# Optimization experiments

Hardware: AMD Instinct MI355X
Metric: run time of the kernel (lower is better)

Reference implementation:

```python
import jax, jax.numpy as jnp
import numpy as np

B, L, D, H, DK, DV, FF, V, N = 1, 1024, 1024, 16, 64, 64, 4096, 32000, 12


def _ln(x, s, b):
    mu = jnp.mean(x, axis=-1, keepdims=True)
    var = jnp.mean((x - mu) ** 2, axis=-1, keepdims=True)
    return (x - mu) / jnp.sqrt(var + 1e-5) * s + b


def _pe(length, d):
    # interleaved sin/cos positional encoding, matching stack([sin,cos],-1).view(L,D)
    i = 2.0 * jnp.arange(d // 2, dtype=jnp.float32)
    base = 10000.0 ** (-i / d)
    half = jnp.arange(length, dtype=jnp.float32)[:, None] * base[None, :]  # [L, D/2]
    return jnp.stack([jnp.sin(half), jnp.cos(half)], axis=-1).reshape(length, d)


def setup_inputs() -> dict:
    key = jax.random.key(0)
    ks = jax.random.split(key, 8)
    s = 0.02
    return {
        "tokens": jax.random.randint(ks[0], (B, L), 0, V),
        "emb": jax.random.normal(ks[1], (V, D), jnp.float32) * s,
        "final_b": jnp.zeros((V,), jnp.float32),
        "Wq": jax.random.normal(ks[2], (N, H, D, DK), jnp.float32) * s,
        "Wk": jax.random.normal(ks[3], (N, H, D, DK), jnp.float32) * s,
        "Wv": jax.random.normal(ks[4], (N, H, D, DV), jnp.float32) * s,
        "Wo": jax.random.normal(ks[5], (N, H * DV, D), jnp.float32) * s,
        "ln1_s": jnp.ones((N, D), jnp.float32),
        "ln1_b": jnp.zeros((N, D), jnp.float32),
        "W1": jax.random.normal(ks[6], (N, D, FF), jnp.float32) * s,
        "b1": jnp.zeros((N, FF), jnp.float32),
        "W2": jax.random.normal(ks[7], (N, FF, D), jnp.float32) * s,
        "b2": jnp.zeros((N, D), jnp.float32),
        "ln2_s": jnp.ones((N, D), jnp.float32),
        "ln2_b": jnp.zeros((N, D), jnp.float32),
    }


def _forward(tokens, emb, final_b, Wq, Wk, Wv, Wo, ln1_s, ln1_b, W1, b1, W2, b2, ln2_s, ln2_b):
    a = emb[tokens] * jnp.sqrt(jnp.float32(3.0 * D))  # tied-weight scaling
    a = a + (a + _pe(L, D))  # faithful to `a += pe(a)` where pe returns x + PE
    mask = jnp.tril(jnp.ones((L, L), dtype=bool))
    scale = 1.0 / jnp.sqrt(jnp.float32(D))  # original divides by sqrt(d_model), not d_k

    def layer(x, p):
        wq, wk, wv, wo, s1, sb1, w1, bb1, w2, bb2, s2, sb2 = p
        q = jnp.einsum('bld,hdk->bhlk', x, wq)
        k = jnp.einsum('bld,hdk->bhlk', x, wk)
        v = jnp.einsum('bld,hdv->bhlv', x, wv)
        scores = jnp.einsum('bhqk,bhmk->bhqm', q, k) * scale  # [B,H,L,L]
        scores = jnp.where(mask, scores, -jnp.inf)  # causal triu(-inf)
        attn = jax.nn.softmax(scores, axis=-1)
        o = jnp.einsum('bhqm,bhmv->bhqv', attn, v)
        o = o.transpose(0, 2, 1, 3).reshape(x.shape[0], L, H * DV)  # concat heads
        x = _ln(x + o @ wo, s1, sb1)  # post-LN residual
        f = jax.nn.relu(x @ w1 + bb1) @ w2 + bb2
        x = _ln(x + f, s2, sb2)
        return x, None

    x, _ = jax.lax.scan(layer, a, (Wq, Wk, Wv, Wo, ln1_s, ln1_b, W1, b1, W2, b2, ln2_s, ln2_b))
    return x @ emb.T + final_b  # tied output projection with bias


def reference(tokens, emb, final_b, Wq, Wk, Wv, Wo, ln1_s, ln1_b, W1, b1, W2, b2, ln2_s, ln2_b):
    return _forward(tokens, emb, final_b, Wq, Wk, Wv, Wo, ln1_s, ln1_b, W1, b1, W2, b2, ln2_s, ln2_b)
```

## Files before the change

### kernel.cpp

```cpp
#include <hip/hip_runtime.h>

typedef unsigned short u16;
typedef __attribute__((ext_vector_type(8))) short short8;
typedef __attribute__((ext_vector_type(4))) float f32x4;
typedef __attribute__((ext_vector_type(4))) u16 u16x4;

#define LSEQ   1024
#define DMODEL 1024
#define NHEAD  16
#define DHEAD  64
#define DFF    4096
#define NLAYER 12
#define NVOCAB 32000

__device__ __forceinline__ u16 f2b(float f) {
  union { float f; unsigned u; } x; x.f = f;
  unsigned r = x.u + 0x7fffu + ((x.u >> 16) & 1u);
  return (u16)(r >> 16);
}

__device__ __forceinline__ f32x4 mfma16(short8 a, short8 b, f32x4 c) {
  return __builtin_amdgcn_mfma_f32_16x16x32_bf16(a, b, c, 0, 0, 0);
}

__device__ __forceinline__ void gload16(const u16* g, u16* l) {
  __builtin_amdgcn_global_load_lds(
      (const __attribute__((address_space(1))) void*)g,
      (__attribute__((address_space(3))) void*)l, 16, 0, 0);
}

template<int N> __device__ __forceinline__ void waitvm() {
  if constexpr (N <= 0)      asm volatile("s_waitcnt vmcnt(0)" ::: "memory");
  else if constexpr (N == 1) asm volatile("s_waitcnt vmcnt(1)" ::: "memory");
  else if constexpr (N == 2) asm volatile("s_waitcnt vmcnt(2)" ::: "memory");
  else if constexpr (N == 3) asm volatile("s_waitcnt vmcnt(3)" ::: "memory");
  else if constexpr (N == 4) asm volatile("s_waitcnt vmcnt(4)" ::: "memory");
  else if constexpr (N == 5) asm volatile("s_waitcnt vmcnt(5)" ::: "memory");
  else if constexpr (N == 6) asm volatile("s_waitcnt vmcnt(6)" ::: "memory");
  else                       asm volatile("s_waitcnt vmcnt(8)" ::: "memory");
}

__global__ __launch_bounds__(256) void embed_k(const int* __restrict__ tok,
    const float* __restrict__ emb, float* __restrict__ x, u16* __restrict__ xb)
{
  const int l = blockIdx.x;
  const int d0 = threadIdx.x * 4;
  const int t = tok[l];
  const float lf = (float)l;
  float o[4]; u16 obv[4];
#pragma unroll
  for (int j = 0; j < 4; ++j) {
    int d = d0 + j;
    int p = d >> 1;
    float ang = lf * powf(10000.0f, -(float)(2 * p) / 1024.0f);
    float pe = (d & 1) ? cosf(ang) : sinf(ang);
    float val = 2.0f * emb[(size_t)t * DMODEL + d] * 55.42562584220407f + pe;
    o[j] = val; obv[j] = f2b(val);
  }
  *reinterpret_cast<float4*>(x + (size_t)l * DMODEL + d0) = make_float4(o[0], o[1], o[2], o[3]);
  u16x4 vb = { obv[0], obv[1], obv[2], obv[3] };
  *reinterpret_cast<u16x4*>(xb + (size_t)l * DMODEL + d0) = vb;
}

__global__ __launch_bounds__(256) void ln_k(const float* __restrict__ xin,
    const float* __restrict__ ypart, int P, const float* __restrict__ ybias,
    const float* __restrict__ s, const float* __restrict__ b,
    float* __restrict__ xout, u16* __restrict__ xbout)
{
  const int row = blockIdx.x, tid = threadIdx.x;
  const int d0 = tid * 4;
  float4 xv = *reinterpret_cast<const float4*>(xin + (size_t)row * DMODEL + d0);
  float t0 = xv.x, t1 = xv.y, t2 = xv.z, t3 = xv.w;
#pragma unroll 2
  for (int p = 0; p < P; ++p) {
    float4 yv = *reinterpret_cast<const float4*>(ypart + (size_t)p * (LSEQ * DMODEL) + (size_t)row * DMODEL + d0);
    t0 += yv.x; t1 += yv.y; t2 += yv.z; t3 += yv.w;
  }
  if (ybias) {
    float4 bb = *reinterpret_cast<const float4*>(ybias + d0);
    t0 += bb.x; t1 += bb.y; t2 += bb.z; t3 += bb.w;
  }
  float sum = t0 + t1 + t2 + t3;
  float sq  = t0 * t0 + t1 * t1 + t2 * t2 + t3 * t3;
#pragma unroll
  for (int d = 1; d < 64; d <<= 1) { sum += __shfl_xor(sum, d); sq += __shfl_xor(sq, d); }
  __shared__ float ssum[4], ssq[4];
  const int wid = tid >> 6;
  if ((tid & 63) == 0) { ssum[wid] = sum; ssq[wid] = sq; }
  __syncthreads();
  sum = ssum[0] + ssum[1] + ssum[2] + ssum[3];
  sq  = ssq[0] + ssq[1] + ssq[2] + ssq[3];
  const float mu = sum * (1.0f / 1024.0f);
  const float var = sq * (1.0f / 1024.0f) - mu * mu;
  const float rstd = rsqrtf(var + 1e-5f);
  float4 sv = *reinterpret_cast<const float4*>(s + d0);
  float4 bv = *reinterpret_cast<const float4*>(b + d0);
  float o0 = (t0 - mu) * rstd * sv.x + bv.x;
  float o1 = (t1 - mu) * rstd * sv.y + bv.y;
  float o2 = (t2 - mu) * rstd * sv.z + bv.z;
  float o3 = (t3 - mu) * rstd * sv.w + bv.w;
  *reinterpret_cast<float4*>(xout + (size_t)row * DMODEL + d0) = make_float4(o0, o1, o2, o3);
  u16x4 vb = { f2b(o0), f2b(o1), f2b(o2), f2b(o3) };
  *reinterpret_cast<u16x4*>(xbout + (size_t)row * DMODEL + d0) = vb;
}

__global__ __launch_bounds__(256) void tconv_k(const float* __restrict__ in, u16* __restrict__ out,
                                               int R, int C, int zper, int lstride, int obase, int zstride)
{
  __shared__ float t[64][65];
  const int rt = blockIdx.y * 64, ct = blockIdx.x * 64;
  const int z = blockIdx.z;
  in += (size_t)z * zstride;
  const int tr = threadIdx.x >> 4, tc = threadIdx.x & 15;
#pragma unroll
  for (int i = 0; i < 4; ++i) {
    int r = i * 16 + tr;
    float4 v = *reinterpret_cast<const float4*>(in + (size_t)(rt + r) * C + ct + tc * 4);
    t[r][tc * 4 + 0] = v.x; t[r][tc * 4 + 1] = v.y;
    t[r][tc * 4 + 2] = v.z; t[r][tc * 4 + 3] = v.w;
  }
  __syncthreads();
  const size_t orow0 = (size_t)(z / zper) * lstride + (size_t)(z % zper) * C + obase + ct;
#pragma unroll
  for (int i = 0; i < 4; ++i) {
    int c = i * 16 + tr;
    u16x4 o;
    o[0] = f2b(t[tc * 4 + 0][c]); o[1] = f2b(t[tc * 4 + 1][c]);
    o[2] = f2b(t[tc * 4 + 2][c]); o[3] = f2b(t[tc * 4 + 3][c]);
    *reinterpret_cast<u16x4*>(out + (orow0 + c) * R + rt + tc * 4) = o;
  }
}

__global__ __launch_bounds__(256) void ec_k(const float* __restrict__ in, u16* __restrict__ out)
{
  const size_t i = ((size_t)blockIdx.x * 256 + threadIdx.x) * 8;
  float4 a = *reinterpret_cast<const float4*>(in + i);
  float4 b = *reinterpret_cast<const float4*>(in + i + 4);
  short8 o;
  o[0] = f2b(a.x); o[1] = f2b(a.y); o[2] = f2b(a.z); o[3] = f2b(a.w);
  o[4] = f2b(b.x); o[5] = f2b(b.y); o[6] = f2b(b.z); o[7] = f2b(b.w);
  *reinterpret_cast<short8*>(out + i) = o;
}

template<int BM, int BN, int BK, int BSRC, bool BIAS, bool RELU, int OUTMODE, int KSPLIT>
__global__ __launch_bounds__(256) void gemm_bt(
    const u16* __restrict__ A, int lda,
    const void* __restrict__ Bp, int ldb,
    const float* __restrict__ bias,
    void* __restrict__ Cv, int ldc, int Ktot)
{
  constexpr int CPR = BK / 8;
  constexpr int SWM = CPR - 1;
  constexpr int LA = (BM * CPR) / 256;
  constexpr int LB = (BN * CPR) / 256;
  constexpr int LT = LA + LB;
  __shared__ u16 As[3][BM * BK];
  __shared__ u16 Bs[3][BN * BK];
  const int tid = threadIdx.x, lane = tid & 63, wid = tid >> 6;
  const int nwg = gridDim.x * gridDim.y;
  const int flat = blockIdx.y * gridDim.x + blockIdx.x;
  const int qq = nwg >> 3;
  const int ni = (flat & 7) * qq + (flat >> 3);
  const int m0 = (ni % gridDim.x) * BM, n0 = (ni / gridDim.x) * BN;
  const int kbase = (KSPLIT > 1) ? blockIdx.z * (Ktot / KSPLIT) : 0;
  const int klen  = (KSPLIT > 1) ? (Ktot / KSPLIT) : Ktot;
  constexpr int FM = BM / 32, FN = BN / 32;
  constexpr int KS = BK / 32;
  const int wm = (wid >> 1) * (BM / 2), wn = (wid & 1) * (BN / 2);
  f32x4 acc[FM][FN] = {};

  if constexpr (BSRC == 0) {
    const u16* Bt = (const u16*)Bp;
    auto stage = [&](int slot, int k0) {
#pragma unroll
      for (int i = 0; i < LA; ++i) {
        int c = i * 256 + tid;
        int row = c / CPR, p0 = c % CPR;
        int part = p0 ^ (((row * CPR) >> 3) & SWM);
        gload16(A + (size_t)(m0 + row) * lda + k0 + part * 8,
                &As[slot][(i * 256 + wid * 64) * 8]);
      }
#pragma unroll
      for (int i = 0; i < LB; ++i) {
        int c = i * 256 + tid;
        int row = c / CPR, p0 = c % CPR;
        int part = p0 ^ (((row * CPR) >> 3) & SWM);
        gload16(Bt + (size_t)(n0 + row) * ldb + k0 + part * 8,
                &Bs[slot][(i * 256 + wid * 64) * 8]);
      }
    };

    const int NT = klen / BK;
    stage(0, kbase);
    stage(1, kbase + BK);
    waitvm<LT>();
    __builtin_amdgcn_s_barrier();
    asm volatile("" ::: "memory");

    int cur = 0, stg = 2;
    for (int t = 0; t < NT; ++t) {
      const bool more = (t + 2 < NT);
      if (more) stage(stg, kbase + (t + 2) * BK);
      asm volatile("" ::: "memory");
      short8 a[KS][FM], b[KS][FN];
#pragma unroll
      for (int ks = 0; ks < KS; ++ks) {
#pragma unroll
        for (int fm = 0; fm < FM; ++fm) {
          int row = wm + fm * 16 + (lane & 15);
          int pidx = (ks * 4 + (lane >> 4)) ^ (((row * CPR) >> 3) & SWM);
          a[ks][fm] = *reinterpret_cast<const short8*>(&As[cur][row * BK + pidx * 8]);
        }
#pragma unroll
        for (int fn = 0; fn < FN; ++fn) {
          int row = wn + fn * 16 + (lane & 15);
          int pidx = (ks * 4 + (lane >> 4)) ^ (((row * CPR) >> 3) & SWM);
          b[ks][fn] = *reinterpret_cast<const short8*>(&Bs[cur][row * BK + pidx * 8]);
        }
      }
#pragma unroll
      for (int ks = 0; ks < KS; ++ks)
#pragma unroll
        for (int fm = 0; fm < FM; ++fm)
#pragma unroll
          for (int fn = 0; fn < FN; ++fn)
            acc[fm][fn] = mfma16(a[ks][fm], b[ks][fn], acc[fm][fn]);
      if (more) waitvm<LT>(); else waitvm<0>();
      __builtin_amdgcn_s_barrier();
      asm volatile("" ::: "memory");
      cur = (cur == 2) ? 0 : cur + 1;
      stg = (stg == 2) ? 0 : stg + 1;
    }
  } else {
    const float* Bf = (const float*)Bp;
    for (int k0 = 0; k0 < Ktot; k0 += BK) {
#pragma unroll
      for (int i = 0; i < LA; ++i) {
        int c = i * 256 + tid;
        int row = c / CPR, part = c % CPR;
        gload16(A + (size_t)(m0 + row) * lda + k0 + part * 8,
                &As[0][(i * 256 + wid * 64) * 8]);
      }
      {
        int row = tid >> 1, kh = (tid & 1) * 16;
        const float* src = Bf + (size_t)(n0 + row) * ldb + k0 + kh;
        float4 v0 = *reinterpret_cast<const float4*>(src);
        float4 v1 = *reinterpret_cast<const float4*>(src + 4);
        float4 v2 = *reinterpret_cast<const float4*>(src + 8);
        float4 v3 = *reinterpret_cast<const float4*>(src + 12);
        short8 p0, p1;
        p0[0] = f2b(v0.x); p0[1] = f2b(v0.y); p0[2] = f2b(v0.z); p0[3] = f2b(v0.w);
        p0[4] = f2b(v1.x); p0[5] = f2b(v1.y); p0[6] = f2b(v1.z); p0[7] = f2b(v1.w);
        p1[0] = f2b(v2.x); p1[1] = f2b(v2.y); p1[2] = f2b(v2.z); p1[3] = f2b(v2.w);
        p1[4] = f2b(v3.x); p1[5] = f2b(v3.y); p1[6] = f2b(v3.z); p1[7] = f2b(v3.w);
        *reinterpret_cast<short8*>(&Bs[0][row * BK + kh])     = p0;
        *reinterpret_cast<short8*>(&Bs[0][row * BK + kh + 8]) = p1;
      }
      __syncthreads();
      short8 a[KS][FM], b[KS][FN];
#pragma unroll
      for (int ks = 0; ks < KS; ++ks) {
#pragma unroll
        for (int fm = 0; fm < FM; ++fm) {
          int row = wm + fm * 16 + (lane & 15);
          a[ks][fm] = *reinterpret_cast<const short8*>(&As[0][row * BK + (ks * 4 + (lane >> 4)) * 8]);
        }
#pragma unroll
        for (int fn = 0; fn < FN; ++fn) {
          int row = wn + fn * 16 + (lane & 15);
          b[ks][fn] = *reinterpret_cast<const short8*>(&Bs[0][row * BK + (ks * 4 + (lane >> 4)) * 8]);
        }
      }
#pragma unroll
      for (int ks = 0; ks < KS; ++ks)
#pragma unroll
        for (int fm = 0; fm < FM; ++fm)
#pragma unroll
          for (int fn = 0; fn < FN; ++fn)
            acc[fm][fn] = mfma16(a[ks][fm], b[ks][fn], acc[fm][fn]);
      __syncthreads();
    }
  }

  const size_t pbase = (KSPLIT > 1) ? (size_t)blockIdx.z * gridDim.x * BM * ldc : 0;
#pragma unroll
  for (int fm = 0; fm < FM; ++fm) {
#pragma unroll
    for (int fn = 0; fn < FN; ++fn) {
#pragma unroll
      for (int r = 0; r < 4; ++r) {
        int row = m0 + wm + fm * 16 + (lane >> 4) * 4 + r;
        int col = n0 + wn + fn * 16 + (lane & 15);
        float val = acc[fm][fn][r];
        if (BIAS) val += bias[col];
        if (RELU) val = fmaxf(val, 0.0f);
        if (OUTMODE == 0) {
          ((float*)Cv)[pbase + (size_t)row * ldc + col] = val;
        } else if (OUTMODE == 1) {
          ((u16*)Cv)[(size_t)row * ldc + col] = f2b(val);
        } else {
          int sel = col >> 10, cc = col & 1023;
          if (sel == 0) val *= 0.03125f;
          ((u16*)Cv)[(size_t)sel * (LSEQ * DMODEL) + (size_t)row * DMODEL + cc] = f2b(val);
        }
      }
    }
  }
}

__global__ __launch_bounds__(256) void attn_k(const u16* __restrict__ q,
    const u16* __restrict__ kmat, const u16* __restrict__ v, u16* __restrict__ o)
{
  __shared__ u16 Ks[64][72];
  __shared__ u16 Vt[64][72];
  __shared__ u16 Pl[4][16][72];
  const int tid = threadIdx.x, lane = tid & 63, wid = tid >> 6;
  const int h = blockIdx.y, qt = blockIdx.x;
  const int qw0 = qt * 64 + wid * 16;
  const int qrow = qw0 + (lane & 15);
  const short8 aq0 = *reinterpret_cast<const short8*>(q + (size_t)qrow * DMODEL + h * DHEAD + (lane >> 4) * 8);
  const short8 aq1 = *reinterpret_cast<const short8*>(q + (size_t)qrow * DMODEL + h * DHEAD + 32 + (lane >> 4) * 8);
  float m_run[4], l_run[4];
  f32x4 oacc[4] = {};
#pragma unroll
  for (int r = 0; r < 4; ++r) { m_run[r] = -1e30f; l_run[r] = 0.0f; }
  const int kvend = qt * 64 + 64;

  const int kvi = tid >> 2, c16 = (tid & 3) * 16;
  short8 kr0, kr1, vr0, vr1;
  auto loadregs = [&](int kv0) {
    const u16* kp = kmat + (size_t)(kv0 + kvi) * DMODEL + h * DHEAD + c16;
    kr0 = *reinterpret_cast<const short8*>(kp);
    kr1 = *reinterpret_cast<const short8*>(kp + 8);
    const u16* vp = v + (size_t)(kv0 + kvi) * DMODEL + h * DHEAD + c16;
    vr0 = *reinterpret_cast<const short8*>(vp);
    vr1 = *reinterpret_cast<const short8*>(vp + 8);
  };
  loadregs(0);

  for (int kv0 = 0; kv0 < kvend; kv0 += 64) {
    __syncthreads();
    *reinterpret_cast<short8*>(&Ks[kvi][c16])     = kr0;
    *reinterpret_cast<short8*>(&Ks[kvi][c16 + 8]) = kr1;
#pragma unroll
    for (int j = 0; j < 8; ++j) { Vt[c16 + j][kvi] = (u16)vr0[j]; Vt[c16 + 8 + j][kvi] = (u16)vr1[j]; }
    __syncthreads();
    if (kv0 + 64 < kvend) loadregs(kv0 + 64);

    float sm[4][4];
#pragma unroll
    for (int t2 = 0; t2 < 4; ++t2) {
      short8 bk0 = *reinterpret_cast<const short8*>(&Ks[t2 * 16 + (lane & 15)][(lane >> 4) * 8]);
      short8 bk1 = *reinterpret_cast<const short8*>(&Ks[t2 * 16 + (lane & 15)][32 + (lane >> 4) * 8]);
      f32x4 s4 = {};
      s4 = mfma16(aq0, bk0, s4);
      s4 = mfma16(aq1, bk1, s4);
#pragma unroll
      for (int r = 0; r < 4; ++r) {
        int rowg = qw0 + (lane >> 4) * 4 + r;
        int colg = kv0 + t2 * 16 + (lane & 15);
        sm[t2][r] = (colg <= rowg) ? s4[r] : -1e30f;
      }
    }
    float alpha[4], p[4][4];
#pragma unroll
    for (int r = 0; r < 4; ++r) {
      float mx = fmaxf(fmaxf(sm[0][r], sm[1][r]), fmaxf(sm[2][r], sm[3][r]));
#pragma unroll
      for (int d = 1; d < 16; d <<= 1) mx = fmaxf(mx, __shfl_xor(mx, d));
      float mn = fmaxf(m_run[r], mx);
      alpha[r] = __expf(m_run[r] - mn);
      float ps = 0.0f;
#pragma unroll
      for (int t2 = 0; t2 < 4; ++t2) { p[t2][r] = __expf(sm[t2][r] - mn); ps += p[t2][r]; }
#pragma unroll
      for (int d = 1; d < 16; d <<= 1) ps += __shfl_xor(ps, d);
      l_run[r] = l_run[r] * alpha[r] + ps;
      m_run[r] = mn;
    }
#pragma unroll
    for (int fn = 0; fn < 4; ++fn) {
      f32x4 t = oacc[fn];
      t[0] *= alpha[0]; t[1] *= alpha[1]; t[2] *= alpha[2]; t[3] *= alpha[3];
      oacc[fn] = t;
    }
#pragma unroll
    for (int r = 0; r < 4; ++r) {
      int rit = (lane >> 4) * 4 + r;
#pragma unroll
      for (int t2 = 0; t2 < 4; ++t2)
        Pl[wid][rit][t2 * 16 + (lane & 15)] = f2b(p[t2][r]);
    }
    short8 pa0 = *reinterpret_cast<const short8*>(&Pl[wid][lane & 15][(lane >> 4) * 8]);
    short8 pa1 = *reinterpret_cast<const short8*>(&Pl[wid][lane & 15][32 + (lane >> 4) * 8]);
#pragma unroll
    for (int fn = 0; fn < 4; ++fn) {
      short8 bv0 = *reinterpret_cast<const short8*>(&Vt[fn * 16 + (lane & 15)][(lane >> 4) * 8]);
      short8 bv1 = *reinterpret_cast<const short8*>(&Vt[fn * 16 + (lane & 15)][32 + (lane >> 4) * 8]);
      oacc[fn] = mfma16(pa0, bv0, oacc[fn]);
      oacc[fn] = mfma16(pa1, bv1, oacc[fn]);
    }
  }
#pragma unroll
  for (int fn = 0; fn < 4; ++fn) {
#pragma unroll
    for (int r = 0; r < 4; ++r) {
      int row = qw0 + (lane >> 4) * 4 + r;
      float val = oacc[fn][r] / l_run[r];
      o[(size_t)row * DMODEL + h * DHEAD + fn * 16 + (lane & 15)] = f2b(val);
    }
  }
}

extern "C" void kernel_launch(void* const* d_in, const int* in_sizes, int n_in,
                              void* d_out, int out_size, void* d_ws, size_t ws_size,
                              hipStream_t stream) {
  (void)in_sizes; (void)n_in; (void)out_size;
  const int*   tok    = (const int*)d_in[0];
  const float* emb    = (const float*)d_in[1];
  const float* finalb = (const float*)d_in[2];
  const float* Wq     = (const float*)d_in[3];
  const float* Wk     = (const float*)d_in[4];
  const float* Wv     = (const float*)d_in[5];
  const float* Wo     = (const float*)d_in[6];
  const float* ln1s   = (const float*)d_in[7];
  const float* ln1b   = (const float*)d_in[8];
  const float* W1     = (const float*)d_in[9];
  const float* b1     = (const float*)d_in[10];
  const float* W2     = (const float*)d_in[11];
  const float* b2     = (const float*)d_in[12];
  const float* ln2s   = (const float*)d_in[13];
  const float* ln2b   = (const float*)d_in[14];
  float* out = (float*)d_out;

  float* x   = (float*)d_ws;
  float* y   = x + LSEQ * DMODEL;
  u16* xb    = (u16*)(y + LSEQ * DMODEL);
  u16* qb    = xb + LSEQ * DMODEL;
  u16* kb    = qb + LSEQ * DMODEL;
  u16* vb    = kb + LSEQ * DMODEL;
  u16* ob    = vb + LSEQ * DMODEL;
  u16* h1    = ob + LSEQ * DMODEL;
  u16* wbase = h1 + LSEQ * DFF;
  float* woPart  = (float*)h1;
  float* ff2Part = (float*)qb;

  const size_t eQKV = (size_t)3 * DMODEL * DMODEL;
  const size_t eWO  = (size_t)DMODEL * DMODEL;
  const size_t eW1  = (size_t)DFF * DMODEL;
  const size_t eW2  = (size_t)DMODEL * DFF;
  const size_t perL = eQKV + eWO + eW1 + eW2;
  const size_t eEMB = (size_t)NVOCAB * DMODEL;
  const size_t actE = (size_t)(wbase - (u16*)d_ws);
  const size_t bigNeed = (actE + NLAYER * perL + eEMB) * 2;
  const size_t midNeed = (actE + perL + eEMB) * 2;
  const int mode = ws_size >= bigNeed ? 2 : (ws_size >= midNeed ? 1 : 0);
  const int WL = (mode == 2) ? NLAYER : 1;

  u16* qkvT = wbase;
  u16* woT  = qkvT + WL * eQKV;
  u16* w1T  = woT  + WL * eWO;
  u16* w2T  = w1T  + WL * eW1;
  u16* embT = w2T  + WL * eW2;

  if (mode == 2) {
    tconv_k<<<dim3(1, 16, 192), 256, 0, stream>>>(Wq, qkvT, DMODEL, DHEAD, 16, 3 * DMODEL, 0,    DMODEL * DHEAD);
    tconv_k<<<dim3(1, 16, 192), 256, 0, stream>>>(Wk, qkvT, DMODEL, DHEAD, 16, 3 * DMODEL, 1024, DMODEL * DHEAD);
    tconv_k<<<dim3(1, 16, 192), 256, 0, stream>>>(Wv, qkvT, DMODEL, DHEAD, 16, 3 * DMODEL, 2048, DMODEL * DHEAD);
    tconv_k<<<dim3(16, 16, 12), 256, 0, stream>>>(Wo, woT, DMODEL, DMODEL, 1, DMODEL, 0, DMODEL * DMODEL);
    tconv_k<<<dim3(64, 16, 12), 256, 0, stream>>>(W1, w1T, DMODEL, DFF, 1, DFF, 0, DMODEL * DFF);
    tconv_k<<<dim3(16, 64, 12), 256, 0, stream>>>(W2, w2T, DFF, DMODEL, 1, DMODEL, 0, DFF * DMODEL);
    ec_k<<<(NVOCAB * DMODEL) / 2048, 256, 0, stream>>>(emb, embT);
  } else if (mode == 1) {
    ec_k<<<(NVOCAB * DMODEL) / 2048, 256, 0, stream>>>(emb, embT);
  }

  embed_k<<<LSEQ, 256, 0, stream>>>(tok, emb, x, xb);

  for (int l = 0; l < NLAYER; ++l) {
    const float* wq  = Wq + (size_t)l * NHEAD * DMODEL * DHEAD;
    const float* wk  = Wk + (size_t)l * NHEAD * DMODEL * DHEAD;
    const float* wv  = Wv + (size_t)l * NHEAD * DMODEL * DHEAD;
    const float* wo  = Wo + (size_t)l * DMODEL * DMODEL;
    const float* w1  = W1 + (size_t)l * DMODEL * DFF;
    const float* b1l = b1 + (size_t)l * DFF;
    const float* w2  = W2 + (size_t)l * DFF * DMODEL;
    const float* b2l = b2 + (size_t)l * DMODEL;
    u16* qkvTl = qkvT + (mode == 2 ? (size_t)l * eQKV : 0);
    u16* woTl  = woT  + (mode == 2 ? (size_t)l * eWO  : 0);
    u16* w1Tl  = w1T  + (mode == 2 ? (size_t)l * eW1  : 0);
    u16* w2Tl  = w2T  + (mode == 2 ? (size_t)l * eW2  : 0);

    if (mode < 2) {
      tconv_k<<<dim3(1, 16, 16), 256, 0, stream>>>(wq, qkvTl, DMODEL, DHEAD, 16, 0, 0,    DMODEL * DHEAD);
      tconv_k<<<dim3(1, 16, 16), 256, 0, stream>>>(wk, qkvTl, DMODEL, DHEAD, 16, 0, 1024, DMODEL * DHEAD);
      tconv_k<<<dim3(1, 16, 16), 256, 0, stream>>>(wv, qkvTl, DMODEL, DHEAD, 16, 0, 2048, DMODEL * DHEAD);
      tconv_k<<<dim3(16, 16, 1), 256, 0, stream>>>(wo, woTl, DMODEL, DMODEL, 1, 0, 0, 0);
      tconv_k<<<dim3(64, 16, 1), 256, 0, stream>>>(w1, w1Tl, DMODEL, DFF, 1, 0, 0, 0);
      tconv_k<<<dim3(16, 64, 1), 256, 0, stream>>>(w2, w2Tl, DFF, DMODEL, 1, 0, 0, 0);
    }

    gemm_bt<128, 128, 32, 0, false, false, 2, 1><<<dim3(8, 24), 256, 0, stream>>>(
        xb, DMODEL, qkvTl, DMODEL, nullptr, qb, DMODEL, DMODEL);
    attn_k<<<dim3(16, 16), 256, 0, stream>>>(qb, kb, vb, ob);
    gemm_bt<128, 64, 32, 0, false, false, 0, 2><<<dim3(8, 16, 2), 256, 0, stream>>>(
        ob, DMODEL, woTl, DMODEL, nullptr, woPart, DMODEL, DMODEL);
    ln_k<<<LSEQ, 256, 0, stream>>>(x, woPart, 2, nullptr,
        ln1s + (size_t)l * DMODEL, ln1b + (size_t)l * DMODEL, x, xb);
    gemm_bt<128, 128, 32, 0, true, true, 1, 1><<<dim3(8, 32), 256, 0, stream>>>(
        xb, DMODEL, w1Tl, DMODEL, b1l, h1, DFF, DMODEL);
    gemm_bt<128, 64, 32, 0, false, false, 0, 2><<<dim3(8, 16, 2), 256, 0, stream>>>(
        h1, DFF, w2Tl, DFF, nullptr, ff2Part, DMODEL, DFF);
    ln_k<<<LSEQ, 256, 0, stream>>>(x, ff2Part, 2, b2l,
        ln2s + (size_t)l * DMODEL, ln2b + (size_t)l * DMODEL, x, xb);
  }

  if (mode >= 1) {
    gemm_bt<128, 128, 32, 0, true, false, 0, 1><<<dim3(8, 250), 256, 0, stream>>>(
        xb, DMODEL, embT, DMODEL, finalb, out, NVOCAB, DMODEL);
  } else {
    gemm_bt<128, 128, 32, 1, true, false, 0, 1><<<dim3(8, 250), 256, 0, stream>>>(
        xb, DMODEL, emb, DMODEL, finalb, out, NVOCAB, DMODEL);
  }
}
```

Baseline: 2.142 ms.

## Load GEMM A operand directly into registers and shrink layer GEMM tiles

The bf16 GEMM path stops staging the A tile in shared memory. Each wave now loads its A fragments from global memory straight into registers, double-buffered across iterations, while B keeps the triple-buffered LDS pipeline. The per-layer GEMMs also switch from 128x128/128x64 tiles with BK=32 to 64x64 tiles with BK=64, which gives many more workgroups to fill the GPU. This saves LDS traffic and space but makes A reads uncoalesced and duplicated across the two N-waves. The unrolled two-iteration loop assumes an even tile count.

```diff
diff --git a/kernel.cpp b/kernel.cpp
--- a/kernel.cpp
+++ b/kernel.cpp
@@ -151,10 +151,10 @@
 {
   constexpr int CPR = BK / 8;
   constexpr int SWM = CPR - 1;
-  constexpr int LA = (BM * CPR) / 256;
   constexpr int LB = (BN * CPR) / 256;
-  constexpr int LT = LA + LB;
-  __shared__ u16 As[3][BM * BK];
+  constexpr int FM = BM / 32, FN = BN / 32;
+  constexpr int KS = BK / 32;
+  constexpr int LAR = KS * FM;
   __shared__ u16 Bs[3][BN * BK];
   const int tid = threadIdx.x, lane = tid & 63, wid = tid >> 6;
   const int nwg = gridDim.x * gridDim.y;
@@ -164,22 +164,12 @@
   const int m0 = (ni % gridDim.x) * BM, n0 = (ni / gridDim.x) * BN;
   const int kbase = (KSPLIT > 1) ? blockIdx.z * (Ktot / KSPLIT) : 0;
   const int klen  = (KSPLIT > 1) ? (Ktot / KSPLIT) : Ktot;
-  constexpr int FM = BM / 32, FN = BN / 32;
-  constexpr int KS = BK / 32;
   const int wm = (wid >> 1) * (BM / 2), wn = (wid & 1) * (BN / 2);
   f32x4 acc[FM][FN] = {};
 
   if constexpr (BSRC == 0) {
     const u16* Bt = (const u16*)Bp;
-    auto stage = [&](int slot, int k0) {
-#pragma unroll
-      for (int i = 0; i < LA; ++i) {
-        int c = i * 256 + tid;
-        int row = c / CPR, p0 = c % CPR;
-        int part = p0 ^ (((row * CPR) >> 3) & SWM);
-        gload16(A + (size_t)(m0 + row) * lda + k0 + part * 8,
-                &As[slot][(i * 256 + wid * 64) * 8]);
-      }
+    auto stageB = [&](int slot, int k0) {
 #pragma unroll
       for (int i = 0; i < LB; ++i) {
         int c = i * 256 + tid;
@@ -189,57 +179,66 @@
                 &Bs[slot][(i * 256 + wid * 64) * 8]);
       }
     };
+    auto loadA = [&](short8 (&dst)[KS][FM], int k0) {
+#pragma unroll
+      for (int ks = 0; ks < KS; ++ks)
+#pragma unroll
+        for (int fm = 0; fm < FM; ++fm) {
+          int row = m0 + wm + fm * 16 + (lane & 15);
+          dst[ks][fm] = *reinterpret_cast<const short8*>(
+              &A[(size_t)row * lda + k0 + (ks * 4 + (lane >> 4)) * 8]);
+        }
+    };
 
     const int NT = klen / BK;
-    stage(0, kbase);
-    stage(1, kbase + BK);
-    waitvm<LT>();
-    __builtin_amdgcn_s_barrier();
-    asm volatile("" ::: "memory");
-
-    int cur = 0, stg = 2;
-    for (int t = 0; t < NT; ++t) {
-      const bool more = (t + 2 < NT);
-      if (more) stage(stg, kbase + (t + 2) * BK);
+    short8 aP[KS][FM], aQ[KS][FM];
+    stageB(0, kbase);
+    if (NT > 1) stageB(1, kbase + BK);
+    loadA(aP, kbase);
+    if (NT > 1) waitvm<LB + LAR>(); else waitvm<LAR>();
+
+    auto iter = [&](int t, short8 (&ac)[KS][FM], short8 (&an)[KS][FM]) {
+      __builtin_amdgcn_s_barrier();
       asm volatile("" ::: "memory");
-      short8 a[KS][FM], b[KS][FN];
-#pragma unroll
-      for (int ks = 0; ks < KS; ++ks) {
-#pragma unroll
-        for (int fm = 0; fm < FM; ++fm) {
-          int row = wm + fm * 16 + (lane & 15);
-          int pidx = (ks * 4 + (lane >> 4)) ^ (((row * CPR) >> 3) & SWM);
-          a[ks][fm] = *reinterpret_cast<const short8*>(&As[cur][row * BK + pidx * 8]);
-        }
+      const bool moreB = (t + 2 < NT), moreA = (t + 1 < NT);
+      const int cur = t % 3, stg = (t + 2) % 3;
+      if (moreB) stageB(stg, kbase + (t + 2) * BK);
+      if (moreA) loadA(an, kbase + (t + 1) * BK);
+      if (moreB)      waitvm<LB + LAR>();
+      else if (moreA) waitvm<LAR>();
+      else            waitvm<0>();
+      short8 b[KS][FN];
+#pragma unroll
+      for (int ks = 0; ks < KS; ++ks)
 #pragma unroll
         for (int fn = 0; fn < FN; ++fn) {
           int row = wn + fn * 16 + (lane & 15);
           int pidx = (ks * 4 + (lane >> 4)) ^ (((row * CPR) >> 3) & SWM);
           b[ks][fn] = *reinterpret_cast<const short8*>(&Bs[cur][row * BK + pidx * 8]);
         }
-      }
 #pragma unroll
       for (int ks = 0; ks < KS; ++ks)
 #pragma unroll
         for (int fm = 0; fm < FM; ++fm)
 #pragma unroll
           for (int fn = 0; fn < FN; ++fn)
-            acc[fm][fn] = mfma16(a[ks][fm], b[ks][fn], acc[fm][fn]);
-      if (more) waitvm<LT>(); else waitvm<0>();
-      __builtin_amdgcn_s_barrier();
-      asm volatile("" ::: "memory");
-      cur = (cur == 2) ? 0 : cur + 1;
-      stg = (stg == 2) ? 0 : stg + 1;
+            acc[fm][fn] = mfma16(ac[ks][fm], b[ks][fn], acc[fm][fn]);
+    };
+
+    for (int t = 0; t < NT; t += 2) {
+      iter(t, aP, aQ);
+      iter(t + 1, aQ, aP);
     }
   } else {
+    __shared__ u16 As_fb[BM * BK];
     const float* Bf = (const float*)Bp;
     for (int k0 = 0; k0 < Ktot; k0 += BK) {
 #pragma unroll
-      for (int i = 0; i < LA; ++i) {
+      for (int i = 0; i < (BM * CPR) / 256; ++i) {
         int c = i * 256 + tid;
         int row = c / CPR, part = c % CPR;
         gload16(A + (size_t)(m0 + row) * lda + k0 + part * 8,
-                &As[0][(i * 256 + wid * 64) * 8]);
+                &As_fb[(i * 256 + wid * 64) * 8]);
       }
       {
         int row = tid >> 1, kh = (tid & 1) * 16;
@@ -263,7 +262,7 @@
 #pragma unroll
         for (int fm = 0; fm < FM; ++fm) {
           int row = wm + fm * 16 + (lane & 15);
-          a[ks][fm] = *reinterpret_cast<const short8*>(&As[0][row * BK + (ks * 4 + (lane >> 4)) * 8]);
+          a[ks][fm] = *reinterpret_cast<const short8*>(&As_fb[row * BK + (ks * 4 + (lane >> 4)) * 8]);
         }
 #pragma unroll
         for (int fn = 0; fn < FN; ++fn) {
@@ -500,16 +499,16 @@
       tconv_k<<<dim3(16, 64, 1), 256, 0, stream>>>(w2, w2Tl, DFF, DMODEL, 1, 0, 0, 0);
     }
 
-    gemm_bt<128, 128, 32, 0, false, false, 2, 1><<<dim3(8, 24), 256, 0, stream>>>(
+    gemm_bt<64, 64, 64, 0, false, false, 2, 1><<<dim3(16, 48), 256, 0, stream>>>(
         xb, DMODEL, qkvTl, DMODEL, nullptr, qb, DMODEL, DMODEL);
     attn_k<<<dim3(16, 16), 256, 0, stream>>>(qb, kb, vb, ob);
-    gemm_bt<128, 64, 32, 0, false, false, 0, 2><<<dim3(8, 16, 2), 256, 0, stream>>>(
+    gemm_bt<64, 64, 64, 0, false, false, 0, 2><<<dim3(16, 16, 2), 256, 0, stream>>>(
         ob, DMODEL, woTl, DMODEL, nullptr, woPart, DMODEL, DMODEL);
     ln_k<<<LSEQ, 256, 0, stream>>>(x, woPart, 2, nullptr,
         ln1s + (size_t)l * DMODEL, ln1b + (size_t)l * DMODEL, x, xb);
-    gemm_bt<128, 128, 32, 0, true, true, 1, 1><<<dim3(8, 32), 256, 0, stream>>>(
+    gemm_bt<64, 64, 64, 0, true, true, 1, 1><<<dim3(16, 64), 256, 0, stream>>>(
         xb, DMODEL, w1Tl, DMODEL, b1l, h1, DFF, DMODEL);
-    gemm_bt<128, 64, 32, 0, false, false, 0, 2><<<dim3(8, 16, 2), 256, 0, stream>>>(
+    gemm_bt<64, 64, 64, 0, false, false, 0, 2><<<dim3(16, 16, 2), 256, 0, stream>>>(
         h1, DFF, w2Tl, DFF, nullptr, ff2Part, DMODEL, DFF);
     ln_k<<<LSEQ, 256, 0, stream>>>(x, ff2Part, 2, b2l,
         ln2s + (size_t)l * DMODEL, ln2b + (size_t)l * DMODEL, x, xb);
```

Measured after the change: 2.215 ms. +3.4%, slower.

## Split-K QKV and FFN1 GEMMs with bf16 partials, shrink tiles elsewhere

Applied to the files above, without the earlier changes.

When the workspace is large enough, the QKV and FFN-up GEMMs use a 2-way K split. Each split writes bf16 partials into a new scratch buffer, and new reduction kernels sum the partials and apply the q-scale or the bias and ReLU. This is meant to raise the block count on the many-CU GPU. The Wo and FFN-down GEMMs, plus the fallback paths, move to 64x64x64 tiles for the same reason. The cost is extra launches and partial-sum traffic, plus an extra bf16 rounding of the partials, which could reduce accuracy.

```diff
diff --git a/kernel.cpp b/kernel.cpp
--- a/kernel.cpp
+++ b/kernel.cpp
@@ -17,6 +17,9 @@
   union { float f; unsigned u; } x; x.f = f;
   unsigned r = x.u + 0x7fffu + ((x.u >> 16) & 1u);
   return (u16)(r >> 16);
+}
+__device__ __forceinline__ float b2f(u16 u) {
+  union { unsigned u; float f; } x; x.u = ((unsigned)u) << 16; return x.f;
 }
 
 __device__ __forceinline__ f32x4 mfma16(short8 a, short8 b, f32x4 c) {
@@ -104,6 +107,39 @@
   *reinterpret_cast<u16x4*>(xbout + (size_t)row * DMODEL + d0) = vb;
 }
 
+__global__ __launch_bounds__(256) void qkvred_k(const u16* __restrict__ sp,
+    u16* __restrict__ q, u16* __restrict__ k, u16* __restrict__ v)
+{
+  const size_t idx = ((size_t)blockIdx.x * 256 + threadIdx.x) * 8;
+  const int row = (int)(idx / 3072), c0 = (int)(idx % 3072);
+  short8 a = *reinterpret_cast<const short8*>(sp + idx);
+  short8 b = *reinterpret_cast<const short8*>(sp + (size_t)LSEQ * 3072 + idx);
+  const int sel = c0 >> 10;
+  const float sc = (sel == 0) ? 0.03125f : 1.0f;
+  short8 o;
+#pragma unroll
+  for (int j = 0; j < 8; ++j)
+    o[j] = (short)f2b((b2f((u16)a[j]) + b2f((u16)b[j])) * sc);
+  u16* dst = (sel == 0 ? q : (sel == 1 ? k : v)) + (size_t)row * DMODEL + (c0 & 1023);
+  *reinterpret_cast<short8*>(dst) = o;
+}
+
+__global__ __launch_bounds__(256) void ffred_k(const u16* __restrict__ sp,
+    const float* __restrict__ bias, u16* __restrict__ out)
+{
+  const size_t idx = ((size_t)blockIdx.x * 256 + threadIdx.x) * 8;
+  const int c0 = (int)(idx % DFF);
+  short8 a = *reinterpret_cast<const short8*>(sp + idx);
+  short8 b = *reinterpret_cast<const short8*>(sp + (size_t)LSEQ * DFF + idx);
+  short8 o;
+#pragma unroll
+  for (int j = 0; j < 8; ++j) {
+    float val = b2f((u16)a[j]) + b2f((u16)b[j]) + bias[c0 + j];
+    o[j] = (short)f2b(fmaxf(val, 0.0f));
+  }
+  *reinterpret_cast<short8*>(out + idx) = o;
+}
+
 __global__ __launch_bounds__(256) void tconv_k(const float* __restrict__ in, u16* __restrict__ out,
                                                int R, int C, int zper, int lstride, int obase, int zstride)
 {
@@ -298,6 +334,8 @@
           ((float*)Cv)[pbase + (size_t)row * ldc + col] = val;
         } else if (OUTMODE == 1) {
           ((u16*)Cv)[(size_t)row * ldc + col] = f2b(val);
+        } else if (OUTMODE == 3) {
+          ((u16*)Cv)[pbase + (size_t)row * ldc + col] = f2b(val);
         } else {
           int sel = col >> 10, cc = col & 1023;
           if (sel == 0) val *= 0.03125f;
@@ -451,8 +489,9 @@
   const size_t eW2  = (size_t)DMODEL * DFF;
   const size_t perL = eQKV + eWO + eW1 + eW2;
   const size_t eEMB = (size_t)NVOCAB * DMODEL;
+  const size_t eSP  = (size_t)2 * LSEQ * DFF;
   const size_t actE = (size_t)(wbase - (u16*)d_ws);
-  const size_t bigNeed = (actE + NLAYER * perL + eEMB) * 2;
+  const size_t bigNeed = (actE + NLAYER * perL + eEMB + eSP) * 2;
   const size_t midNeed = (actE + perL + eEMB) * 2;
   const int mode = ws_size >= bigNeed ? 2 : (ws_size >= midNeed ? 1 : 0);
   const int WL = (mode == 2) ? NLAYER : 1;
@@ -462,6 +501,7 @@
   u16* w1T  = woT  + WL * eWO;
   u16* w2T  = w1T  + WL * eW1;
   u16* embT = w2T  + WL * eW2;
+  u16* sp   = embT + eEMB;
 
   if (mode == 2) {
     tconv_k<<<dim3(1, 16, 192), 256, 0, stream>>>(Wq, qkvT, DMODEL, DHEAD, 16, 3 * DMODEL, 0,    DMODEL * DHEAD);
@@ -500,16 +540,28 @@
       tconv_k<<<dim3(16, 64, 1), 256, 0, stream>>>(w2, w2Tl, DFF, DMODEL, 1, 0, 0, 0);
     }
 
-    gemm_bt<128, 128, 32, 0, false, false, 2, 1><<<dim3(8, 24), 256, 0, stream>>>(
-        xb, DMODEL, qkvTl, DMODEL, nullptr, qb, DMODEL, DMODEL);
+    if (mode == 2) {
+      gemm_bt<128, 128, 32, 0, false, false, 3, 2><<<dim3(8, 24, 2), 256, 0, stream>>>(
+          xb, DMODEL, qkvTl, DMODEL, nullptr, sp, 3 * DMODEL, DMODEL);
+      qkvred_k<<<(LSEQ * 3 * DMODEL) / 2048, 256, 0, stream>>>(sp, qb, kb, vb);
+    } else {
+      gemm_bt<64, 64, 64, 0, false, false, 2, 1><<<dim3(16, 48), 256, 0, stream>>>(
+          xb, DMODEL, qkvTl, DMODEL, nullptr, qb, DMODEL, DMODEL);
+    }
     attn_k<<<dim3(16, 16), 256, 0, stream>>>(qb, kb, vb, ob);
-    gemm_bt<128, 64, 32, 0, false, false, 0, 2><<<dim3(8, 16, 2), 256, 0, stream>>>(
+    gemm_bt<64, 64, 64, 0, false, false, 0, 2><<<dim3(16, 16, 2), 256, 0, stream>>>(
         ob, DMODEL, woTl, DMODEL, nullptr, woPart, DMODEL, DMODEL);
     ln_k<<<LSEQ, 256, 0, stream>>>(x, woPart, 2, nullptr,
         ln1s + (size_t)l * DMODEL, ln1b + (size_t)l * DMODEL, x, xb);
-    gemm_bt<128, 128, 32, 0, true, true, 1, 1><<<dim3(8, 32), 256, 0, stream>>>(
-        xb, DMODEL, w1Tl, DMODEL, b1l, h1, DFF, DMODEL);
-    gemm_bt<128, 64, 32, 0, false, false, 0, 2><<<dim3(8, 16, 2), 256, 0, stream>>>(
+    if (mode == 2) {
+      gemm_bt<128, 128, 32, 0, false, false, 3, 2><<<dim3(8, 32, 2), 256, 0, stream>>>(
+          xb, DMODEL, w1Tl, DMODEL, nullptr, sp, DFF, DMODEL);
+      ffred_k<<<(LSEQ * DFF) / 2048, 256, 0, stream>>>(sp, b1l, h1);
+    } else {
+      gemm_bt<64, 64, 64, 0, true, true, 1, 1><<<dim3(16, 64), 256, 0, stream>>>(
+          xb, DMODEL, w1Tl, DMODEL, b1l, h1, DFF, DMODEL);
+    }
+    gemm_bt<64, 64, 64, 0, false, false, 0, 2><<<dim3(16, 16, 2), 256, 0, stream>>>(
         h1, DFF, w2Tl, DFF, nullptr, ff2Part, DMODEL, DFF);
     ln_k<<<LSEQ, 256, 0, stream>>>(x, ff2Part, 2, b2l,
         ln2s + (size_t)l * DMODEL, ln2b + (size_t)l * DMODEL, x, xb);
```

Result: faster. 1.890 ms (-11.8%).
